# Kernel tuning notes

Hardware: AMD Instinct MI355X
Metric: run time of the kernel (lower is better)

## Reference

```python
import jax, jax.numpy as jnp
import numpy as np

FACTOR = 50
IN_CHANNELS = 512

def setup_inputs() -> dict:
    key = jax.random.key(0)
    ks = jax.random.split(key, 9)
    B, Cin, W, H = 16, 256, 64, 64
    D = 512  # out_channels
    L = W * H
    U = FACTOR * int(np.ceil(np.log(L)))  # 450
    return {
        "input_1": jax.random.normal(ks[0], (B, Cin, W, H), jnp.float32),
        "input_2": jax.random.normal(ks[1], (B, Cin, W, H), jnp.float32),
        "Wq": jax.random.normal(ks[2], (D, 2 * Cin), jnp.float32) * 0.02,
        "bq": jax.random.normal(ks[3], (D,), jnp.float32) * 0.02,
        "Wk": jax.random.normal(ks[4], (D, 2 * Cin), jnp.float32) * 0.02,
        "bk": jax.random.normal(ks[5], (D,), jnp.float32) * 0.02,
        "Wv": jax.random.normal(ks[6], (D, 2 * Cin), jnp.float32) * 0.02,
        "bv": jax.random.normal(ks[7], (D,), jnp.float32) * 0.02,
        "idx_sample": jax.random.randint(ks[8], (U,), 0, L, jnp.int32),
    }

def reference(input_1, input_2, Wq, bq, Wk, bk, Wv, bv, idx_sample):
    x = jnp.concatenate([input_1, input_2], axis=1)  # [B, 2*Cin, W, H]
    B, C, Wd, Ht = x.shape
    L = Wd * Ht
    D = Wq.shape[0]
    # 1x1 convs == per-pixel channel matmul; then torch's raw .view to [B,1,L,D]
    def proj(Wm, bm):
        y = jnp.einsum('bchw,oc->bohw', x, Wm) + bm[None, :, None, None]
        return y.reshape(B, 1, L, D)  # memory reinterpretation, as in torch .view
    q = proj(Wq, bq)
    k = proj(Wk, bk)
    v = proj(Wv, bv)

    u = min(FACTOR * int(np.ceil(np.log(L))), L)  # n_top == sample_k here
    # sampled Q-K scores
    K_sample = k[:, :, idx_sample, :]                      # [B,1,U,D]
    QKs = jnp.einsum('bhld,bhsd->bhls', q, K_sample)       # [B,1,L,U]
    M = QKs.max(-1) - QKs.sum(-1) / L                      # sparsity measure [B,1,L]
    M_top = jax.lax.top_k(M, u)[1]                         # [B,1,u]
    Q_reduce = jnp.take_along_axis(q, M_top[..., None], axis=2)  # [B,1,u,D]
    scores = jnp.einsum('bhud,bhld->bhul', Q_reduce, k)    # [B,1,u,L]
    scores = scores * (1.0 / IN_CHANNELS ** 0.5)

    # initial context: mean of V broadcast over queries
    context = jnp.broadcast_to(v.mean(axis=2, keepdims=True), (B, 1, L, D))
    attn = jax.nn.softmax(scores, axis=-1)                 # [B,1,u,L]
    upd = jnp.einsum('bhul,bhld->bhud', attn, v)           # [B,1,u,D]
    bI = jnp.arange(B)[:, None, None]
    hI = jnp.arange(1)[None, :, None]
    context = context.at[bI, hI, M_top].set(upd)
    # transpose(2,1) then torch .view to [B, D, W, H]
    out = context.transpose(0, 2, 1, 3).reshape(B, D, Wd, Ht)
    return out
```

## Files before the change

kernel.cpp:

```cpp
#include <hip/hip_runtime.h>
#include <cstdint>
#include <cstddef>

#define L_DIM 4096
#define D_DIM 512
#define CIN   256
#define BATCH 16
#define KSPLIT 4

typedef _Float16 half8 __attribute__((ext_vector_type(8)));
typedef unsigned short ushort8 __attribute__((ext_vector_type(8)));
typedef float f32x4 __attribute__((ext_vector_type(4)));

__device__ __forceinline__ void gld16(const _Float16* g, _Float16* l) {
    __builtin_amdgcn_global_load_lds(
        (const __attribute__((address_space(1))) unsigned int*)g,
        (__attribute__((address_space(3))) unsigned int*)l,
        16, 0, 0);
}

__global__ __launch_bounds__(256) void convert_w(
    const float* __restrict__ Wq, const float* __restrict__ Wk,
    const float* __restrict__ Wv,
    _Float16* __restrict__ Wh, _Float16* __restrict__ Wl)
{
    const int w = blockIdx.y;
    const float* src = (w == 0) ? Wq : (w == 1) ? Wk : Wv;
    int i = blockIdx.x * 256 + threadIdx.x;
    float xv = src[i];
    _Float16 hi = (_Float16)xv;
    Wh[(size_t)w * 262144 + i] = hi;
    Wl[(size_t)w * 262144 + i] = (_Float16)(xv - (float)hi);
}

__global__ __launch_bounds__(256) void convert_x(
    const float* __restrict__ x1, const float* __restrict__ x2,
    _Float16* __restrict__ XTh, _Float16* __restrict__ XTl, int phase)
{
    const int bb = blockIdx.z;
    const int b = phase * 8 + bb;
    const int s0 = blockIdx.x * 64;
    const int c0 = blockIdx.y * 64;
    __shared__ float t[64][65];
    const int tid = threadIdx.x;
    const int g = tid >> 6, sy = tid & 63;
    const float* src = (c0 < CIN)
        ? (x1 + (size_t)b * CIN * L_DIM + (size_t)c0 * L_DIM)
        : (x2 + (size_t)b * CIN * L_DIM + (size_t)(c0 - CIN) * L_DIM);
    #pragma unroll
    for (int r = 0; r < 16; r++) {
        int cl = g * 16 + r;
        t[cl][sy] = src[(size_t)cl * L_DIM + s0 + sy];
    }
    __syncthreads();
    _Float16* outh = XTh + (size_t)bb * L_DIM * 512 + (size_t)s0 * 512 + c0;
    _Float16* outl = XTl + (size_t)bb * L_DIM * 512 + (size_t)s0 * 512 + c0;
    #pragma unroll
    for (int r = 0; r < 16; r++) {
        int sl = g * 16 + r;
        float xv = t[sy][sl];
        _Float16 hi = (_Float16)xv;
        float lo = xv - (float)hi;
        outh[(size_t)sl * 512 + sy] = hi;
        outl[(size_t)sl * 512 + sy] = (_Float16)lo;
    }
}

__global__ __launch_bounds__(256) void proj_mfma_qk(
    const _Float16* __restrict__ Wh, const _Float16* __restrict__ Wl,
    const _Float16* __restrict__ XTh, const _Float16* __restrict__ XTl,
    const float* __restrict__ bq, const float* __restrict__ bk,
    _Float16* __restrict__ qh, _Float16* __restrict__ ql,
    _Float16* __restrict__ kh, _Float16* __restrict__ kl,
    int phase)
{
    const int z = blockIdx.z;
    const int bb = z >> 1, w = z & 1;
    const int b = phase * 8 + bb;
    const _Float16* Ah_g = Wh + (size_t)w * 262144;
    const _Float16* Al_g = Wl + (size_t)w * 262144;
    const _Float16* Bh_g = XTh + (size_t)bb * ((size_t)L_DIM * 512);
    const _Float16* Bl_g = XTl + (size_t)bb * ((size_t)L_DIM * 512);
    const float* bias = (w == 0) ? bq : bk;
    _Float16* outh = ((w == 0) ? qh : kh) + (size_t)b * ((size_t)D_DIM * L_DIM);
    _Float16* outl = ((w == 0) ? ql : kl) + (size_t)b * ((size_t)D_DIM * L_DIM);

    const int m0 = blockIdx.y * 128;
    const int n0 = blockIdx.x * 128;

    __shared__ _Float16 lds[4 * 128 * 32];
    _Float16* ldsA_h = lds;
    _Float16* ldsA_l = lds + 4096;
    _Float16* ldsB_h = lds + 8192;
    _Float16* ldsB_l = lds + 12288;

    const int tid = threadIdx.x;
    const int w4 = tid >> 6, lane = tid & 63;
    const int lr = lane & 15, quad = lane >> 4;
    const int wr = w4 >> 1, wc = w4 & 1;

    f32x4 acc[4][4] = {};

    const int q1 = w4 * 128 + lane, q2 = q1 + 64;
    const int r1 = q1 >> 2, c41 = (q1 & 3) ^ ((r1 >> 1) & 3);
    const int r2 = q2 >> 2, c42 = (q2 & 3) ^ ((r2 >> 1) & 3);

    const _Float16* pAh1 = Ah_g + (size_t)(m0 + r1) * 512 + c41 * 8;
    const _Float16* pAh2 = Ah_g + (size_t)(m0 + r2) * 512 + c42 * 8;
    const _Float16* pAl1 = Al_g + (size_t)(m0 + r1) * 512 + c41 * 8;
    const _Float16* pAl2 = Al_g + (size_t)(m0 + r2) * 512 + c42 * 8;
    const _Float16* pBh1 = Bh_g + (size_t)(n0 + r1) * 512 + c41 * 8;
    const _Float16* pBh2 = Bh_g + (size_t)(n0 + r2) * 512 + c42 * 8;
    const _Float16* pBl1 = Bl_g + (size_t)(n0 + r1) * 512 + c41 * 8;
    const _Float16* pBl2 = Bl_g + (size_t)(n0 + r2) * 512 + c42 * 8;

    _Float16* d1 = (_Float16*)(lds) + (size_t)(w4 * 128) * 8;
    _Float16* d2 = (_Float16*)(lds) + (size_t)(w4 * 128 + 64) * 8;

    const int qsw = (quad ^ ((lr >> 1) & 3)) * 8;

    for (int k0 = 0; k0 < 512; k0 += 32) {
        if (k0) __syncthreads();
        gld16(pAh1 + k0, d1);
        gld16(pAh2 + k0, d2);
        gld16(pAl1 + k0, d1 + 4096);
        gld16(pAl2 + k0, d2 + 4096);
        gld16(pBh1 + k0, d1 + 8192);
        gld16(pBh2 + k0, d2 + 8192);
        gld16(pBl1 + k0, d1 + 12288);
        gld16(pBl2 + k0, d2 + 12288);
        __syncthreads();

        half8 fAh[4], fAl[4];
        #pragma unroll
        for (int i = 0; i < 4; i++) {
            int m = wr * 64 + i * 16 + lr;
            fAh[i] = *(const half8*)(ldsA_h + m * 32 + qsw);
            fAl[i] = *(const half8*)(ldsA_l + m * 32 + qsw);
        }
        #pragma unroll
        for (int j = 0; j < 4; j++) {
            int n = wc * 64 + j * 16 + lr;
            half8 fBh = *(const half8*)(ldsB_h + n * 32 + qsw);
            half8 fBl = *(const half8*)(ldsB_l + n * 32 + qsw);
            #pragma unroll
            for (int i = 0; i < 4; i++) {
                acc[i][j] = __builtin_amdgcn_mfma_f32_16x16x32_f16(fAh[i], fBh, acc[i][j], 0, 0, 0);
                acc[i][j] = __builtin_amdgcn_mfma_f32_16x16x32_f16(fAl[i], fBh, acc[i][j], 0, 0, 0);
                acc[i][j] = __builtin_amdgcn_mfma_f32_16x16x32_f16(fAh[i], fBl, acc[i][j], 0, 0, 0);
            }
        }
    }

    #pragma unroll
    for (int i = 0; i < 4; i++) {
        int mg = m0 + wr * 64 + i * 16 + quad * 4;
        #pragma unroll
        for (int r = 0; r < 4; r++) {
            float bvv = bias[mg + r];
            #pragma unroll
            for (int j = 0; j < 4; j++) {
                int ng = n0 + wc * 64 + j * 16 + lr;
                float val = acc[i][j][r] + bvv;
                _Float16 hi = (_Float16)val;
                size_t off = (size_t)(mg + r) * L_DIM + ng;
                outh[off] = hi;
                outl[off] = (_Float16)(val - (float)hi);
            }
        }
    }
}

__global__ __launch_bounds__(256) void proj_mfma_v(
    const _Float16* __restrict__ Wh, const _Float16* __restrict__ XTh,
    const float* __restrict__ bv, _Float16* __restrict__ vh, int phase)
{
    const int bb = blockIdx.z;
    const int b = phase * 8 + bb;
    const _Float16* Ah_g = Wh + (size_t)2 * 262144;
    const _Float16* Bh_g = XTh + (size_t)bb * ((size_t)L_DIM * 512);
    _Float16* outh = vh + (size_t)b * ((size_t)D_DIM * L_DIM);

    const int m0 = blockIdx.y * 128;
    const int n0 = blockIdx.x * 128;

    __shared__ _Float16 lds[2 * 128 * 32];
    _Float16* ldsA_h = lds;
    _Float16* ldsB_h = lds + 4096;

    const int tid = threadIdx.x;
    const int w4 = tid >> 6, lane = tid & 63;
    const int lr = lane & 15, quad = lane >> 4;
    const int wr = w4 >> 1, wc = w4 & 1;

    f32x4 acc[4][4] = {};

    const int q1 = w4 * 128 + lane, q2 = q1 + 64;
    const int r1 = q1 >> 2, c41 = (q1 & 3) ^ ((r1 >> 1) & 3);
    const int r2 = q2 >> 2, c42 = (q2 & 3) ^ ((r2 >> 1) & 3);

    const _Float16* pAh1 = Ah_g + (size_t)(m0 + r1) * 512 + c41 * 8;
    const _Float16* pAh2 = Ah_g + (size_t)(m0 + r2) * 512 + c42 * 8;
    const _Float16* pBh1 = Bh_g + (size_t)(n0 + r1) * 512 + c41 * 8;
    const _Float16* pBh2 = Bh_g + (size_t)(n0 + r2) * 512 + c42 * 8;

    _Float16* d1 = (_Float16*)(lds) + (size_t)(w4 * 128) * 8;
    _Float16* d2 = (_Float16*)(lds) + (size_t)(w4 * 128 + 64) * 8;

    const int qsw = (quad ^ ((lr >> 1) & 3)) * 8;

    for (int k0 = 0; k0 < 512; k0 += 32) {
        if (k0) __syncthreads();
        gld16(pAh1 + k0, d1);
        gld16(pAh2 + k0, d2);
        gld16(pBh1 + k0, d1 + 4096);
        gld16(pBh2 + k0, d2 + 4096);
        __syncthreads();

        half8 fAh[4];
        #pragma unroll
        for (int i = 0; i < 4; i++) {
            int m = wr * 64 + i * 16 + lr;
            fAh[i] = *(const half8*)(ldsA_h + m * 32 + qsw);
        }
        #pragma unroll
        for (int j = 0; j < 4; j++) {
            int n = wc * 64 + j * 16 + lr;
            half8 fBh = *(const half8*)(ldsB_h + n * 32 + qsw);
            #pragma unroll
            for (int i = 0; i < 4; i++)
                acc[i][j] = __builtin_amdgcn_mfma_f32_16x16x32_f16(fAh[i], fBh, acc[i][j], 0, 0, 0);
        }
    }

    #pragma unroll
    for (int i = 0; i < 4; i++) {
        int mg = m0 + wr * 64 + i * 16 + quad * 4;
        #pragma unroll
        for (int r = 0; r < 4; r++) {
            float bvv = bv[mg + r];
            #pragma unroll
            for (int j = 0; j < 4; j++) {
                int ng = n0 + wc * 64 + j * 16 + lr;
                outh[(size_t)(mg + r) * L_DIM + ng] = (_Float16)(acc[i][j][r] + bvv);
            }
        }
    }
}

__global__ __launch_bounds__(256) void qks_mfma(
    const _Float16* __restrict__ qh, const _Float16* __restrict__ ql,
    const _Float16* __restrict__ kh, const _Float16* __restrict__ kl,
    const int* __restrict__ idx_sample,
    float* __restrict__ Mmax, float* __restrict__ Msum, int U, int nst)
{
    const int b = blockIdx.z;
    const int stile = blockIdx.y;
    const int l0 = blockIdx.x * 128;
    const int s0 = stile * 128;
    const size_t perB = (size_t)D_DIM * L_DIM;
    const _Float16* qh_b = qh + (size_t)b * perB;
    const _Float16* ql_b = ql + (size_t)b * perB;
    const _Float16* kh_b = kh + (size_t)b * perB;
    const _Float16* kl_b = kl + (size_t)b * perB;

    __shared__ _Float16 ldsAh[4096], ldsAl[4096];
    __shared__ _Float16 ldsBh[4096], ldsBl[4096];
    __shared__ int sidx[128];
    __shared__ float redm[8][128];
    __shared__ float reds[8][128];

    const int tid = threadIdx.x;
    const int w4 = tid >> 6, lane = tid & 63;
    const int lr = lane & 15, quad = lane >> 4;
    const int ws = w4 >> 1, wl = w4 & 1;

    if (tid < 128) {
        int s = s0 + tid;
        sidx[tid] = (s < U) ? idx_sample[s] : idx_sample[0];
    }
    __syncthreads();

    f32x4 acc[4][4] = {};
    const int qsw = (quad ^ ((lr >> 1) & 3)) * 8;

    for (int k0 = 0; k0 < 512; k0 += 32) {
        #pragma unroll
        for (int t = 0; t < 2; t++) {
            int c = w4 * 128 + t * 64 + lane;
            int row = c >> 2, part = (c & 3) ^ ((row >> 1) & 3);
            int krow = sidx[row];
            size_t go = (size_t)krow * 512 + k0 + part * 8;
            size_t qo = (size_t)(l0 + row) * 512 + k0 + part * 8;
            int base = (w4 * 128 + t * 64) * 8;
            gld16(kh_b + go, ldsAh + base);
            gld16(kl_b + go, ldsAl + base);
            gld16(qh_b + qo, ldsBh + base);
            gld16(ql_b + qo, ldsBl + base);
        }
        __syncthreads();

        half8 fAh[4], fAl[4];
        #pragma unroll
        for (int i = 0; i < 4; i++) {
            int s = ws * 64 + i * 16 + lr;
            fAh[i] = *(const half8*)(ldsAh + s * 32 + qsw);
            fAl[i] = *(const half8*)(ldsAl + s * 32 + qsw);
        }
        #pragma unroll
        for (int j = 0; j < 4; j++) {
            int l = wl * 64 + j * 16 + lr;
            half8 fBh = *(const half8*)(ldsBh + l * 32 + qsw);
            half8 fBl = *(const half8*)(ldsBl + l * 32 + qsw);
            #pragma unroll
            for (int i = 0; i < 4; i++) {
                acc[i][j] = __builtin_amdgcn_mfma_f32_16x16x32_f16(fAh[i], fBh, acc[i][j], 0, 0, 0);
                acc[i][j] = __builtin_amdgcn_mfma_f32_16x16x32_f16(fAl[i], fBh, acc[i][j], 0, 0, 0);
                acc[i][j] = __builtin_amdgcn_mfma_f32_16x16x32_f16(fAh[i], fBl, acc[i][j], 0, 0, 0);
            }
        }
        __syncthreads();
    }

    float runmax[4], runsum[4];
    #pragma unroll
    for (int j = 0; j < 4; j++) { runmax[j] = -__builtin_inff(); runsum[j] = 0.f; }
    #pragma unroll
    for (int i = 0; i < 4; i++) {
        #pragma unroll
        for (int r = 0; r < 4; r++) {
            int sg = s0 + ws * 64 + i * 16 + quad * 4 + r;
            if (sg < U) {
                #pragma unroll
                for (int j = 0; j < 4; j++) {
                    runmax[j] = fmaxf(runmax[j], acc[i][j][r]);
                    runsum[j] += acc[i][j][r];
                }
            }
        }
    }
    #pragma unroll
    for (int j = 0; j < 4; j++) {
        int l = wl * 64 + j * 16 + lr;
        redm[ws * 4 + quad][l] = runmax[j];
        reds[ws * 4 + quad][l] = runsum[j];
    }
    __syncthreads();
    if (tid < 128) {
        float gm = -__builtin_inff(), gs = 0.f;
        #pragma unroll
        for (int t = 0; t < 8; t++) { gm = fmaxf(gm, redm[t][tid]); gs += reds[t][tid]; }
        size_t o = ((size_t)b * nst + stile) * L_DIM + l0 + tid;
        Mmax[o] = gm;
        Msum[o] = gs;
    }
}

__global__ __launch_bounds__(512) void topk_select(
    const float* __restrict__ Mmax, const float* __restrict__ Msum,
    int* __restrict__ topidx, int U, int nst)
{
    const int b = blockIdx.x;
    const int tid = threadIdx.x;
    __shared__ int wcnt[8];
    __shared__ int basec;

    unsigned mykey[8];
    #pragma unroll
    for (int t = 0; t < 8; t++) {
        int l = t * 512 + tid;
        float gm = -__builtin_inff(), gs = 0.f;
        for (int st = 0; st < nst; st++) {
            size_t o = ((size_t)b * nst + st) * L_DIM + l;
            gm = fmaxf(gm, Mmax[o]);
            gs += Msum[o];
        }
        float M = gm - gs * (1.f / (float)L_DIM);
        unsigned bits = __float_as_uint(M);
        mykey[t] = (bits & 0x80000000u) ? ~bits : (bits | 0x80000000u);
    }
    if (tid == 0) basec = 0;

    const int wv = tid >> 6, lane = tid & 63;
    unsigned lo = 0u, hi = 0xFFFFFFFFu;
    while (lo < hi) {
        unsigned hl = hi - lo;
        unsigned mid = lo + (hl >> 1) + (hl & 1u);
        int c = 0;
        #pragma unroll
        for (int t = 0; t < 8; t++) c += (mykey[t] >= mid) ? 1 : 0;
        #pragma unroll
        for (int o = 32; o > 0; o >>= 1) c += __shfl_down(c, o, 64);
        if (lane == 0) wcnt[wv] = c;
        __syncthreads();
        int total = 0;
        #pragma unroll
        for (int i = 0; i < 8; i++) total += wcnt[i];
        if (total >= U) lo = mid; else hi = mid - 1;
        __syncthreads();
    }
    #pragma unroll
    for (int t = 0; t < 8; t++) {
        if (mykey[t] >= lo) {
            int pos = atomicAdd(&basec, 1);
            if (pos < U) topidx[b * U + pos] = t * 512 + tid;
        }
    }
}

__global__ __launch_bounds__(512) void vmean_partial(
    const _Float16* __restrict__ vh, float* __restrict__ partial)
{
    const int ch = blockIdx.x, b = blockIdx.y;
    const int d = threadIdx.x;
    const _Float16* vhb = vh + (size_t)b * ((size_t)D_DIM * L_DIM);
    float acc = 0.f;
    const int lbeg = ch * 128;
    for (int l = lbeg; l < lbeg + 128; l++)
        acc += (float)vhb[(size_t)l * D_DIM + d];
    partial[((size_t)b * 32 + ch) * D_DIM + d] = acc;
}

__global__ __launch_bounds__(512) void vmean_reduce(const float* __restrict__ partial,
                                                    float* __restrict__ vmean)
{
    const int b = blockIdx.x;
    const int d = threadIdx.x;
    float acc = 0.f;
    for (int ch = 0; ch < 32; ch++) acc += partial[((size_t)b * 32 + ch) * D_DIM + d];
    vmean[b * D_DIM + d] = acc * (1.f / (float)L_DIM);
}

__global__ __launch_bounds__(256) void fill_out(const float* __restrict__ vmean,
                                                float* __restrict__ out)
{
    const int z = blockIdx.x;
    const int b = z >> 6, lch = z & 63;
    __shared__ float vm[512];
    vm[threadIdx.x] = vmean[b * 512 + threadIdx.x];
    vm[threadIdx.x + 256] = vmean[b * 512 + threadIdx.x + 256];
    __syncthreads();
    float* op = out + (size_t)b * ((size_t)D_DIM * L_DIM) + (size_t)lch * 64 * 512;
    #pragma unroll
    for (int it = 0; it < 32; it++) {
        int flat = (threadIdx.x + it * 256) * 4;
        int d = flat & 511;
        float4 r = { vm[d], vm[d + 1], vm[d + 2], vm[d + 3] };
        *(float4*)&op[flat] = r;
    }
}

__global__ __launch_bounds__(256) void zero_sel(const int* __restrict__ topidx,
                                                float* __restrict__ out, int U)
{
    const int u = blockIdx.x, b = blockIdx.y;
    int row = topidx[b * U + u];
    float2 z = { 0.f, 0.f };
    *(float2*)&out[(size_t)b * ((size_t)D_DIM * L_DIM) + (size_t)row * 512
                   + threadIdx.x * 2] = z;
}

__global__ __launch_bounds__(256) void scores_mfma(
    const _Float16* __restrict__ qh, const _Float16* __restrict__ kh,
    const int* __restrict__ topidx,
    _Float16* __restrict__ sh, int U)
{
    const int b = blockIdx.z;
    const int s0 = blockIdx.x * 128;
    const int u0 = blockIdx.y * 128;
    const size_t perB = (size_t)D_DIM * L_DIM;
    const _Float16* qh_b = qh + (size_t)b * perB;
    const _Float16* kh_b = kh + (size_t)b * perB;
    _Float16* sh_b = sh + (size_t)b * (size_t)U * L_DIM;

    __shared__ _Float16 ldsAh[4096];
    __shared__ _Float16 ldsBh[4096];
    __shared__ int arow[128];

    const int tid = threadIdx.x;
    const int w4 = tid >> 6, lane = tid & 63;
    const int lr = lane & 15, quad = lane >> 4;
    const int wu = w4 >> 1, wn = w4 & 1;

    if (tid < 128) {
        int u = u0 + tid;
        arow[tid] = topidx[b * U + (u < U ? u : U - 1)];
    }
    __syncthreads();

    f32x4 acc[4][4] = {};
    const int qsw = (quad ^ ((lr >> 1) & 3)) * 8;

    for (int k0 = 0; k0 < 512; k0 += 32) {
        #pragma unroll
        for (int t = 0; t < 2; t++) {
            int c = w4 * 128 + t * 64 + lane;
            int row = c >> 2, part = (c & 3) ^ ((row >> 1) & 3);
            size_t go = (size_t)arow[row] * 512 + k0 + part * 8;
            size_t ko = (size_t)(s0 + row) * 512 + k0 + part * 8;
            int base = (w4 * 128 + t * 64) * 8;
            gld16(qh_b + go, ldsAh + base);
            gld16(kh_b + ko, ldsBh + base);
        }
        __syncthreads();

        half8 fAh[4];
        #pragma unroll
        for (int i = 0; i < 4; i++) {
            int u = wu * 64 + i * 16 + lr;
            fAh[i] = *(const half8*)(ldsAh + u * 32 + qsw);
        }
        #pragma unroll
        for (int j = 0; j < 4; j++) {
            int s = wn * 64 + j * 16 + lr;
            half8 fBh = *(const half8*)(ldsBh + s * 32 + qsw);
            #pragma unroll
            for (int i = 0; i < 4; i++)
                acc[i][j] = __builtin_amdgcn_mfma_f32_16x16x32_f16(fAh[i], fBh, acc[i][j], 0, 0, 0);
        }
        __syncthreads();
    }

    const float scale = 0.044194173824159216f;
    #pragma unroll
    for (int i = 0; i < 4; i++) {
        #pragma unroll
        for (int r = 0; r < 4; r++) {
            int u = u0 + wu * 64 + i * 16 + quad * 4 + r;
            if (u < U) {
                #pragma unroll
                for (int j = 0; j < 4; j++) {
                    int s = s0 + wn * 64 + j * 16 + lr;
                    sh_b[(size_t)u * L_DIM + s] = (_Float16)(acc[i][j][r] * scale);
                }
            }
        }
    }
}

__global__ __launch_bounds__(256) void softmax_h(_Float16* __restrict__ sh)
{
    _Float16* hrow = sh + (size_t)blockIdx.x * L_DIM;
    const int tid = threadIdx.x;
    float x[16];
    #pragma unroll
    for (int t = 0; t < 2; t++) {
        half8 h8 = *(const half8*)(hrow + tid * 8 + t * 2048);
        #pragma unroll
        for (int i = 0; i < 8; i++) x[t * 8 + i] = (float)h8[i];
    }
    __shared__ float red[256];
    float lm = -__builtin_inff();
    #pragma unroll
    for (int i = 0; i < 16; i++) lm = fmaxf(lm, x[i]);
    red[tid] = lm;
    __syncthreads();
    for (int o = 128; o > 0; o >>= 1) {
        if (tid < o) red[tid] = fmaxf(red[tid], red[tid + o]);
        __syncthreads();
    }
    float m = red[0];
    __syncthreads();
    float ls = 0.f;
    #pragma unroll
    for (int i = 0; i < 16; i++) { x[i] = __expf(x[i] - m); ls += x[i]; }
    red[tid] = ls;
    __syncthreads();
    for (int o = 128; o > 0; o >>= 1) {
        if (tid < o) red[tid] += red[tid + o];
        __syncthreads();
    }
    float inv = 1.f / red[0];
    #pragma unroll
    for (int t = 0; t < 2; t++) {
        half8 h8;
        #pragma unroll
        for (int i = 0; i < 8; i++) h8[i] = (_Float16)(x[t * 8 + i] * inv);
        *(half8*)(hrow + tid * 8 + t * 2048) = h8;
    }
}

__global__ __launch_bounds__(256) void upd_mfma(
    const _Float16* __restrict__ sh, const _Float16* __restrict__ vh,
    const int* __restrict__ topidx, float* __restrict__ out, int U)
{
    const int zz = blockIdx.z;
    const int b = zz >> 2, ks = zz & 3;
    const int n0 = blockIdx.y * 128;
    const int u0 = blockIdx.x * 128;
    const size_t perB = (size_t)D_DIM * L_DIM;
    const _Float16* ah_b = sh + (size_t)b * (size_t)U * L_DIM;
    const _Float16* vh_b = vh + (size_t)b * perB;

    __shared__ _Float16 ldsAh[4096];
    __shared__ _Float16 ldsBh[4096];

    const int tid = threadIdx.x;
    const int w4 = tid >> 6, lane = tid & 63;
    const int lr = lane & 15, quad = lane >> 4;
    const int wu = w4 >> 1, wd = w4 & 1;

    const int part = tid & 15, spair = tid >> 4;
    const int s_b = spair * 2;
    const int colw = ((spair >> 2) + part) & 3;
    const int so2 = (s_b & 7);

    f32x4 acc[4][4] = {};
    const int qsw = (quad ^ ((lr >> 1) & 3)) * 8;

    const int kbeg = ks * (L_DIM / KSPLIT);
    const int kend = kbeg + (L_DIM / KSPLIT);
    for (int k0 = kbeg; k0 < kend; k0 += 32) {
        #pragma unroll
        for (int t = 0; t < 2; t++) {
            int c = w4 * 128 + t * 64 + lane;
            int u = c >> 2, pt = (c & 3) ^ ((u >> 1) & 3);
            int urow = u0 + u; if (urow >= U) urow = U - 1;
            size_t ao = (size_t)urow * L_DIM + k0 + pt * 8;
            int base = (w4 * 128 + t * 64) * 8;
            gld16(ah_b + ao, ldsAh + base);
        }
        {
            const _Float16* s0p = vh_b + (size_t)(k0 + s_b) * 512 + n0 + part * 8;
            const _Float16* s1p = s0p + 512;
            ushort8 a0 = *(const ushort8*)s0p;
            ushort8 a1 = *(const ushort8*)s1p;
            #pragma unroll
            for (int t = 0; t < 8; t++) {
                int dd = part * 8 + t;
                unsigned int ph = (unsigned int)a0[t] | ((unsigned int)a1[t] << 16);
                *(unsigned int*)(ldsBh + dd * 32 + colw * 8 + so2) = ph;
            }
        }
        __syncthreads();

        half8 fAh[4];
        #pragma unroll
        for (int i = 0; i < 4; i++) {
            int u = wu * 64 + i * 16 + lr;
            fAh[i] = *(const half8*)(ldsAh + u * 32 + qsw);
        }
        #pragma unroll
        for (int j = 0; j < 4; j++) {
            int dd = wd * 64 + j * 16 + lr;
            int col = (quad + (dd >> 3)) & 3;
            half8 fBh = *(const half8*)(ldsBh + dd * 32 + col * 8);
            #pragma unroll
            for (int i = 0; i < 4; i++)
                acc[i][j] = __builtin_amdgcn_mfma_f32_16x16x32_f16(fAh[i], fBh, acc[i][j], 0, 0, 0);
        }
        __syncthreads();
    }

    #pragma unroll
    for (int i = 0; i < 4; i++) {
        #pragma unroll
        for (int r = 0; r < 4; r++) {
            int u = u0 + wu * 64 + i * 16 + quad * 4 + r;
            if (u < U) {
                int lrow = topidx[b * U + u];
                #pragma unroll
                for (int j = 0; j < 4; j++) {
                    int dd = n0 + wd * 64 + j * 16 + lr;
                    unsafeAtomicAdd(&out[(size_t)b * perB + (size_t)lrow * 512 + dd],
                                    acc[i][j][r]);
                }
            }
        }
    }
}

extern "C" void kernel_launch(void* const* d_in, const int* in_sizes, int n_in,
                              void* d_out, int out_size, void* d_ws, size_t ws_size,
                              hipStream_t stream)
{
    const float* x1 = (const float*)d_in[0];
    const float* x2 = (const float*)d_in[1];
    const float* Wq = (const float*)d_in[2];
    const float* bq = (const float*)d_in[3];
    const float* Wk = (const float*)d_in[4];
    const float* bk = (const float*)d_in[5];
    const float* Wv = (const float*)d_in[6];
    const float* bv = (const float*)d_in[7];
    const int*  idx = (const int*)d_in[8];
    const int U = in_sizes[8];
    const int nst = (U + 127) / 128;

    float* out = (float*)d_out;

    const size_t perB = (size_t)D_DIM * L_DIM;
    const size_t tenH = (size_t)BATCH * perB;
    _Float16* qh = (_Float16*)d_ws;
    _Float16* ql = qh + tenH;
    _Float16* kh = ql + tenH;
    _Float16* kl = kh + tenH;
    _Float16* vh = kl + tenH;
    float* S = (float*)(vh + tenH);

    _Float16* XTh = (_Float16*)S;
    _Float16* XTl = XTh + (size_t)8 * L_DIM * 512;
    _Float16* Wh  = XTl + (size_t)8 * L_DIM * 512;
    _Float16* Wl  = Wh + (size_t)3 * 512 * 512;

    _Float16* sh = (_Float16*)S;
    float* vmean = (float*)(sh + (size_t)BATCH * (size_t)U * L_DIM);
    float* partU = vmean + (size_t)BATCH * D_DIM;
    float* vpart = partU;
    float* Mmax  = partU;
    float* Msum  = Mmax + (size_t)BATCH * nst * L_DIM;
    int* topidx  = (int*)(partU + (size_t)2 * BATCH * 4 * L_DIM);

    convert_w<<<dim3(1024, 3), 256, 0, stream>>>(Wq, Wk, Wv, Wh, Wl);

    for (int phase = 0; phase < 2; phase++) {
        convert_x<<<dim3(64, 8, 8), 256, 0, stream>>>(x1, x2, XTh, XTl, phase);
        proj_mfma_qk<<<dim3(L_DIM / 128, D_DIM / 128, 8 * 2), 256, 0, stream>>>(
            Wh, Wl, XTh, XTl, bq, bk, qh, ql, kh, kl, phase);
        proj_mfma_v<<<dim3(L_DIM / 128, D_DIM / 128, 8), 256, 0, stream>>>(
            Wh, XTh, bv, vh, phase);
    }

    vmean_partial<<<dim3(32, BATCH), 512, 0, stream>>>(vh, vpart);
    vmean_reduce<<<BATCH, 512, 0, stream>>>(vpart, vmean);
    fill_out<<<BATCH * 64, 256, 0, stream>>>(vmean, out);

    qks_mfma<<<dim3(L_DIM / 128, nst, BATCH), 256, 0, stream>>>(
        qh, ql, kh, kl, idx, Mmax, Msum, U, nst);
    topk_select<<<BATCH, 512, 0, stream>>>(Mmax, Msum, topidx, U, nst);

    const int utiles = (U + 127) / 128;
    scores_mfma<<<dim3(L_DIM / 128, utiles, BATCH), 256, 0, stream>>>(
        qh, kh, topidx, sh, U);
    softmax_h<<<BATCH * U, 256, 0, stream>>>(sh);
    zero_sel<<<dim3(U, BATCH), 256, 0, stream>>>(topidx, out, U);
    upd_mfma<<<dim3(utiles, D_DIM / 128, BATCH * KSPLIT), 256, 0, stream>>>(
        sh, vh, topidx, out, U);
}
```

Before: 883.8 us.

## Two-pass top-k: coarse fp16 sample scores, then split-precision refine on candidates

```diff
diff --git a/kernel.cpp b/kernel.cpp
--- a/kernel.cpp
+++ b/kernel.cpp
@@ -7,6 +7,8 @@
 #define CIN   256
 #define BATCH 16
 #define KSPLIT 4
+#define CANDMAX 2048
+#define CAND_MARGIN 0.06f
 
 typedef _Float16 half8 __attribute__((ext_vector_type(8)));
 typedef unsigned short ushort8 __attribute__((ext_vector_type(8)));
@@ -248,9 +250,8 @@
     }
 }
 
-__global__ __launch_bounds__(256) void qks_mfma(
-    const _Float16* __restrict__ qh, const _Float16* __restrict__ ql,
-    const _Float16* __restrict__ kh, const _Float16* __restrict__ kl,
+__global__ __launch_bounds__(256) void qks_x1(
+    const _Float16* __restrict__ qh, const _Float16* __restrict__ kh,
     const int* __restrict__ idx_sample,
     float* __restrict__ Mmax, float* __restrict__ Msum, int U, int nst)
 {
@@ -260,12 +261,10 @@
     const int s0 = stile * 128;
     const size_t perB = (size_t)D_DIM * L_DIM;
     const _Float16* qh_b = qh + (size_t)b * perB;
-    const _Float16* ql_b = ql + (size_t)b * perB;
     const _Float16* kh_b = kh + (size_t)b * perB;
-    const _Float16* kl_b = kl + (size_t)b * perB;
-
-    __shared__ _Float16 ldsAh[4096], ldsAl[4096];
-    __shared__ _Float16 ldsBh[4096], ldsBl[4096];
+
+    __shared__ _Float16 ldsAh[4096];
+    __shared__ _Float16 ldsBh[4096];
     __shared__ int sidx[128];
     __shared__ float redm[8][128];
     __shared__ float reds[8][128];
@@ -292,6 +291,171 @@
             int krow = sidx[row];
             size_t go = (size_t)krow * 512 + k0 + part * 8;
             size_t qo = (size_t)(l0 + row) * 512 + k0 + part * 8;
+            int base = (w4 * 128 + t * 64) * 8;
+            gld16(kh_b + go, ldsAh + base);
+            gld16(qh_b + qo, ldsBh + base);
+        }
+        __syncthreads();
+
+        half8 fAh[4];
+        #pragma unroll
+        for (int i = 0; i < 4; i++) {
+            int s = ws * 64 + i * 16 + lr;
+            fAh[i] = *(const half8*)(ldsAh + s * 32 + qsw);
+        }
+        #pragma unroll
+        for (int j = 0; j < 4; j++) {
+            int l = wl * 64 + j * 16 + lr;
+            half8 fBh = *(const half8*)(ldsBh + l * 32 + qsw);
+            #pragma unroll
+            for (int i = 0; i < 4; i++)
+                acc[i][j] = __builtin_amdgcn_mfma_f32_16x16x32_f16(fAh[i], fBh, acc[i][j], 0, 0, 0);
+        }
+        __syncthreads();
+    }
+
+    float runmax[4], runsum[4];
+    #pragma unroll
+    for (int j = 0; j < 4; j++) { runmax[j] = -__builtin_inff(); runsum[j] = 0.f; }
+    #pragma unroll
+    for (int i = 0; i < 4; i++) {
+        #pragma unroll
+        for (int r = 0; r < 4; r++) {
+            int sg = s0 + ws * 64 + i * 16 + quad * 4 + r;
+            if (sg < U) {
+                #pragma unroll
+                for (int j = 0; j < 4; j++) {
+                    runmax[j] = fmaxf(runmax[j], acc[i][j][r]);
+                    runsum[j] += acc[i][j][r];
+                }
+            }
+        }
+    }
+    #pragma unroll
+    for (int j = 0; j < 4; j++) {
+        int l = wl * 64 + j * 16 + lr;
+        redm[ws * 4 + quad][l] = runmax[j];
+        reds[ws * 4 + quad][l] = runsum[j];
+    }
+    __syncthreads();
+    if (tid < 128) {
+        float gm = -__builtin_inff(), gs = 0.f;
+        #pragma unroll
+        for (int t = 0; t < 8; t++) { gm = fmaxf(gm, redm[t][tid]); gs += reds[t][tid]; }
+        size_t o = ((size_t)b * nst + stile) * L_DIM + l0 + tid;
+        Mmax[o] = gm;
+        Msum[o] = gs;
+    }
+}
+
+__global__ __launch_bounds__(512) void topk_cand(
+    const float* __restrict__ Mmax, const float* __restrict__ Msum,
+    int* __restrict__ candlist, int* __restrict__ ncand, int U, int nst)
+{
+    const int b = blockIdx.x;
+    const int tid = threadIdx.x;
+    __shared__ int wcnt[8];
+    __shared__ int basec;
+
+    float Mv[8];
+    unsigned mykey[8];
+    #pragma unroll
+    for (int t = 0; t < 8; t++) {
+        int l = t * 512 + tid;
+        float gm = -__builtin_inff(), gs = 0.f;
+        for (int st = 0; st < nst; st++) {
+            size_t o = ((size_t)b * nst + st) * L_DIM + l;
+            gm = fmaxf(gm, Mmax[o]);
+            gs += Msum[o];
+        }
+        float M = gm - gs * (1.f / (float)L_DIM);
+        Mv[t] = M;
+        unsigned bits = __float_as_uint(M);
+        mykey[t] = (bits & 0x80000000u) ? ~bits : (bits | 0x80000000u);
+    }
+    if (tid == 0) basec = 0;
+
+    const int wv = tid >> 6, lane = tid & 63;
+    unsigned lo = 0u, hi = 0xFFFFFFFFu;
+    while (lo < hi) {
+        unsigned hl = hi - lo;
+        unsigned mid = lo + (hl >> 1) + (hl & 1u);
+        int c = 0;
+        #pragma unroll
+        for (int t = 0; t < 8; t++) c += (mykey[t] >= mid) ? 1 : 0;
+        #pragma unroll
+        for (int o = 32; o > 0; o >>= 1) c += __shfl_down(c, o, 64);
+        if (lane == 0) wcnt[wv] = c;
+        __syncthreads();
+        int total = 0;
+        #pragma unroll
+        for (int i = 0; i < 8; i++) total += wcnt[i];
+        if (total >= U) lo = mid; else hi = mid - 1;
+        __syncthreads();
+    }
+    unsigned tb = (lo & 0x80000000u) ? (lo & 0x7FFFFFFFu) : ~lo;
+    float Tval = __uint_as_float(tb) - CAND_MARGIN;
+    #pragma unroll
+    for (int t = 0; t < 8; t++) {
+        if (Mv[t] >= Tval) {
+            int pos = atomicAdd(&basec, 1);
+            if (pos < CANDMAX) candlist[b * CANDMAX + pos] = t * 512 + tid;
+        }
+    }
+    __syncthreads();
+    if (tid == 0) ncand[b] = (basec < CANDMAX) ? basec : CANDMAX;
+}
+
+__global__ __launch_bounds__(256) void refine_mfma(
+    const _Float16* __restrict__ qh, const _Float16* __restrict__ ql,
+    const _Float16* __restrict__ kh, const _Float16* __restrict__ kl,
+    const int* __restrict__ idx_sample, const int* __restrict__ candlist,
+    const int* __restrict__ ncand,
+    float* __restrict__ Rmax, float* __restrict__ Rsum, int U, int nst)
+{
+    const int b = blockIdx.z;
+    const int nc = ncand[b];
+    const int c0 = blockIdx.x * 128;
+    if (c0 >= nc) return;
+    const int stile = blockIdx.y;
+    const int s0 = stile * 128;
+    const size_t perB = (size_t)D_DIM * L_DIM;
+    const _Float16* qh_b = qh + (size_t)b * perB;
+    const _Float16* ql_b = ql + (size_t)b * perB;
+    const _Float16* kh_b = kh + (size_t)b * perB;
+    const _Float16* kl_b = kl + (size_t)b * perB;
+
+    __shared__ _Float16 ldsAh[4096], ldsAl[4096];
+    __shared__ _Float16 ldsBh[4096], ldsBl[4096];
+    __shared__ int sidx[128];
+    __shared__ int crow[128];
+    __shared__ float redm[8][128];
+    __shared__ float reds[8][128];
+
+    const int tid = threadIdx.x;
+    const int w4 = tid >> 6, lane = tid & 63;
+    const int lr = lane & 15, quad = lane >> 4;
+    const int ws = w4 >> 1, wl = w4 & 1;
+
+    if (tid < 128) {
+        int s = s0 + tid;
+        sidx[tid] = (s < U) ? idx_sample[s] : idx_sample[0];
+        int c = c0 + tid;
+        crow[tid] = candlist[b * CANDMAX + (c < nc ? c : 0)];
+    }
+    __syncthreads();
+
+    f32x4 acc[4][4] = {};
+    const int qsw = (quad ^ ((lr >> 1) & 3)) * 8;
+
+    for (int k0 = 0; k0 < 512; k0 += 32) {
+        #pragma unroll
+        for (int t = 0; t < 2; t++) {
+            int c = w4 * 128 + t * 64 + lane;
+            int row = c >> 2, part = (c & 3) ^ ((row >> 1) & 3);
+            int krow = sidx[row];
+            size_t go = (size_t)krow * 512 + k0 + part * 8;
+            size_t qo = (size_t)crow[row] * 512 + k0 + part * 8;
             int base = (w4 * 128 + t * 64) * 8;
             gld16(kh_b + go, ldsAh + base);
             gld16(kl_b + go, ldsAl + base);
@@ -350,32 +514,37 @@
         float gm = -__builtin_inff(), gs = 0.f;
         #pragma unroll
         for (int t = 0; t < 8; t++) { gm = fmaxf(gm, redm[t][tid]); gs += reds[t][tid]; }
-        size_t o = ((size_t)b * nst + stile) * L_DIM + l0 + tid;
-        Mmax[o] = gm;
-        Msum[o] = gs;
-    }
-}
-
-__global__ __launch_bounds__(512) void topk_select(
-    const float* __restrict__ Mmax, const float* __restrict__ Msum,
+        size_t o = ((size_t)b * nst + stile) * CANDMAX + c0 + tid;
+        Rmax[o] = gm;
+        Rsum[o] = gs;
+    }
+}
+
+__global__ __launch_bounds__(512) void topk_final(
+    const float* __restrict__ Rmax, const float* __restrict__ Rsum,
+    const int* __restrict__ candlist, const int* __restrict__ ncand,
     int* __restrict__ topidx, int U, int nst)
 {
     const int b = blockIdx.x;
     const int tid = threadIdx.x;
     __shared__ int wcnt[8];
     __shared__ int basec;
-
-    unsigned mykey[8];
-    #pragma unroll
-    for (int t = 0; t < 8; t++) {
-        int l = t * 512 + tid;
-        float gm = -__builtin_inff(), gs = 0.f;
-        for (int st = 0; st < nst; st++) {
-            size_t o = ((size_t)b * nst + st) * L_DIM + l;
-            gm = fmaxf(gm, Mmax[o]);
-            gs += Msum[o];
-        }
-        float M = gm - gs * (1.f / (float)L_DIM);
+    const int nc = ncand[b];
+
+    unsigned mykey[4];
+    #pragma unroll
+    for (int t = 0; t < 4; t++) {
+        int c = t * 512 + tid;
+        float M = -__builtin_inff();
+        if (c < nc) {
+            float gm = -__builtin_inff(), gs = 0.f;
+            for (int st = 0; st < nst; st++) {
+                size_t o = ((size_t)b * nst + st) * CANDMAX + c;
+                gm = fmaxf(gm, Rmax[o]);
+                gs += Rsum[o];
+            }
+            M = gm - gs * (1.f / (float)L_DIM);
+        }
         unsigned bits = __float_as_uint(M);
         mykey[t] = (bits & 0x80000000u) ? ~bits : (bits | 0x80000000u);
     }
@@ -388,7 +557,7 @@
         unsigned mid = lo + (hl >> 1) + (hl & 1u);
         int c = 0;
         #pragma unroll
-        for (int t = 0; t < 8; t++) c += (mykey[t] >= mid) ? 1 : 0;
+        for (int t = 0; t < 4; t++) c += (mykey[t] >= mid) ? 1 : 0;
         #pragma unroll
         for (int o = 32; o > 0; o >>= 1) c += __shfl_down(c, o, 64);
         if (lane == 0) wcnt[wv] = c;
@@ -400,10 +569,10 @@
         __syncthreads();
     }
     #pragma unroll
-    for (int t = 0; t < 8; t++) {
+    for (int t = 0; t < 4; t++) {
         if (mykey[t] >= lo) {
             int pos = atomicAdd(&basec, 1);
-            if (pos < U) topidx[b * U + pos] = t * 512 + tid;
+            if (pos < U) topidx[b * U + pos] = candlist[b * CANDMAX + t * 512 + tid];
         }
     }
 }
@@ -708,7 +877,11 @@
     float* vpart = partU;
     float* Mmax  = partU;
     float* Msum  = Mmax + (size_t)BATCH * nst * L_DIM;
-    int* topidx  = (int*)(partU + (size_t)2 * BATCH * 4 * L_DIM);
+    int* topidx   = (int*)(Msum + (size_t)BATCH * nst * L_DIM);
+    int* candlist = topidx + BATCH * 512;
+    int* ncand    = candlist + BATCH * CANDMAX;
+    float* Rmax   = (float*)(ncand + 64);
+    float* Rsum   = Rmax + (size_t)BATCH * nst * CANDMAX;
 
     convert_w<<<dim3(1024, 3), 256, 0, stream>>>(Wq, Wk, Wv, Wh, Wl);
 
@@ -724,9 +897,12 @@
     vmean_reduce<<<BATCH, 512, 0, stream>>>(vpart, vmean);
     fill_out<<<BATCH * 64, 256, 0, stream>>>(vmean, out);
 
-    qks_mfma<<<dim3(L_DIM / 128, nst, BATCH), 256, 0, stream>>>(
-        qh, ql, kh, kl, idx, Mmax, Msum, U, nst);
-    topk_select<<<BATCH, 512, 0, stream>>>(Mmax, Msum, topidx, U, nst);
+    qks_x1<<<dim3(L_DIM / 128, nst, BATCH), 256, 0, stream>>>(
+        qh, kh, idx, Mmax, Msum, U, nst);
+    topk_cand<<<BATCH, 512, 0, stream>>>(Mmax, Msum, candlist, ncand, U, nst);
+    refine_mfma<<<dim3(CANDMAX / 128, nst, BATCH), 256, 0, stream>>>(
+        qh, ql, kh, kl, idx, candlist, ncand, Rmax, Rsum, U, nst);
+    topk_final<<<BATCH, 512, 0, stream>>>(Rmax, Rsum, candlist, ncand, topidx, U, nst);
 
     const int utiles = (U + 127) / 128;
     scores_mfma<<<dim3(L_DIM / 128, utiles, BATCH), 256, 0, stream>>>(
```

Measured after the change: 913.9 us. 1.03x slower.
